# Performance work log

Measured on AMD Instinct MI355X. Metric: run time of the kernel, lower is better.

The kernel has to match this reference:

```python
import jax, jax.numpy as jnp
import numpy as np

NUM_CLASSES = 80
ALPHA = 0.25
GAMMA = 2.0
CONF_T = 0.5
IOU_T = 0.5
N_ANCHORS = 6144


def _pairwise_iou(b):
    # b: [n,4] (x1,y1,x2,y2) -> [n,n] IoU matrix
    area = (b[:, 2] - b[:, 0]) * (b[:, 3] - b[:, 1])
    lt = jnp.maximum(b[:, None, :2], b[None, :, :2])
    rb = jnp.minimum(b[:, None, 2:], b[None, :, 2:])
    wh = jnp.clip(rb - lt, 0.0)
    inter = wh[..., 0] * wh[..., 1]
    return inter / (area[:, None] + area[None, :] - inter)


def _nms(boxes, scores, thr):
    # torchvision-style NMS: returns kept indices in decreasing-score order
    order = jnp.argsort(-scores)
    iou = _pairwise_iou(boxes[order])
    n = boxes.shape[0]
    ar = jnp.arange(n)
    def body(i, supp):
        return supp | ((iou[i] > thr) & (ar > i) & jnp.logical_not(supp[i]))
    supp = jax.lax.fori_loop(0, n, body, jnp.zeros(n, dtype=bool))
    kept_pos = jnp.where(~supp)[0]  # eager: concrete shapes
    return order[kept_pos]


def _make_boxes(tb, floc):
    # tb: [1,1,4] target box; floc: [Nf,2] filtered predicted locations
    # replicates loc_determined with T=1: (tx1*px, ty1*py, tx2*px, ty2*py)
    px, py = floc[:, 0], floc[:, 1]
    return jnp.stack([tb[0, 0, 0] * px, tb[0, 0, 1] * py,
                      tb[0, 0, 2] * px, tb[0, 0, 3] * py], axis=1)


def _smooth_l1_sum(pred, tgt):
    d = jnp.abs(pred - tgt)  # broadcasts [k,C,4] vs [1,1,4]
    return jnp.where(d < 1.0, 0.5 * d * d, d - 0.5).sum()


def setup_inputs() -> dict:
    key = jax.random.key(0)
    k1, k2, k3 = jax.random.split(key, 3)
    locations = jax.random.uniform(k1, (1, N_ANCHORS, 2), dtype=jnp.float32)
    confidences = jax.random.uniform(k2, (1, N_ANCHORS, NUM_CLASSES), dtype=jnp.float32)
    # valid target box (x1<x2, y1<y2) in [0,1]
    target_boxes = jnp.array([[[0.15, 0.2, 0.85, 0.9]]], dtype=jnp.float32)
    target_labels = jax.random.randint(k3, (1,), 0, NUM_CLASSES)
    return {"locations": locations, "confidences": confidences,
            "target_boxes": target_boxes, "target_labels": target_labels}


def reference(locations, confidences, target_boxes, target_labels):
    conf = confidences[0]                       # [N,C]
    scores_max = conf.max(axis=1)
    idx_f = jnp.where(scores_max > CONF_T)[0]   # eager boolean filter
    if idx_f.shape[0] == 0:
        return jnp.float32(0.001)
    floc = locations[0, idx_f, :]               # [Nf,2]
    fconf = conf[idx_f]                         # [Nf,C]
    boxes = _make_boxes(target_boxes, floc)     # [Nf,4] (pred_loc_final)
    score = fconf[:, 0]                         # class-0 score, as in original
    keep = _nms(boxes, score, IOU_T)            # kept indices
    if keep.shape[0] == 0:
        return jnp.float32(0.001)
    matched_loc = boxes[keep]                   # [M,4]
    matched_conf = fconf[keep]                  # [M,C]
    k = target_labels.shape[0]                  # = 1
    topv, topi = jax.lax.top_k(matched_conf.T, k)  # per-class top-k over dim 0
    topv, topi = topv.T, topi.T                 # [k,C]
    pred_bin = (topv[:, 0] > 0.5).astype(jnp.float32)  # [k]
    mloc = matched_loc[topi]                    # [k,C,4]
    loc_loss = _smooth_l1_sum(mloc, target_boxes)
    # F.cross_entropy with 1-D float input/target = probabilities mode, unbatched
    ce = -(target_labels.astype(jnp.float32) * jax.nn.log_softmax(pred_bin)).sum()
    focal = ALPHA * (1.0 - jnp.exp(-ce)) ** GAMMA * ce
    # original bug preserved: num_positives = sum of kept *indices*
    num_pos = keep.sum().astype(jnp.float32)
    return (loc_loss + focal) / num_pos
```

## Files before the change

kernel.cpp:

```cpp
#include <hip/hip_runtime.h>
#include <stdint.h>

#define N_ANCHORS 6144
#define NUM_CLASSES 80
#define NWORDS 96
#define NTILES 24
#define SCAN_B 32
#define ROWSTRIDE 128

__device__ unsigned long long g_mask[(size_t)N_ANCHORS * NWORDS + 64];
__device__ float4 g_sbox[N_ANCHORS];
__device__ int    g_rpart[NTILES][N_ANCHORS];
__device__ int    g_fpart[NTILES][N_ANCHORS];
__device__ int    g_sAnchor[N_ANCHORS];
__device__ int    g_sFi[N_ANCHORS];
__device__ int    g_keptPos[N_ANCHORS];
__device__ int    g_F, g_K, g_np, g_done;
__device__ float  g_loss;

__device__ __forceinline__ float anchor_key(const float* __restrict__ conf, int i, bool& valid) {
    const float4* cp4 = (const float4*)(conf + (size_t)i * NUM_CLASSES);
    float4 v0 = cp4[0];
    float score = v0.x;
    float m = fmaxf(fmaxf(v0.x, v0.y), fmaxf(v0.z, v0.w));
    #pragma unroll
    for (int c = 1; c < NUM_CLASSES / 4; ++c) {
        float4 v = cp4[c];
        m = fmaxf(m, fmaxf(fmaxf(v.x, v.y), fmaxf(v.z, v.w)));
    }
    valid = m > 0.5f;
    return valid ? score : -1.0f;
}

__global__ void __launch_bounds__(256) k_rank(const float* __restrict__ conf) {
    __shared__ float skey[256];
    int y = blockIdx.y;
    int j0 = y * 256;
    bool vj;
    skey[threadIdx.x] = anchor_key(conf, j0 + threadIdx.x, vj);
    int i = blockIdx.x * 256 + threadIdx.x;
    bool vi;
    float ki = anchor_key(conf, i, vi);
    __syncthreads();
    int r = 0, f = 0;
    #pragma unroll 8
    for (int jj = 0; jj < 256; ++jj) {
        float kj = skey[jj];
        int j = j0 + jj;
        bool valid_j = kj >= 0.0f;
        r += (kj > ki) || (kj == ki && j < i && valid_j);
        f += (j < i) && valid_j;
    }
    g_rpart[y][i] = r;
    g_fpart[y][i] = f;
}

__global__ void __launch_bounds__(256) k_scatter(const float* __restrict__ loc,
                                                 const float* __restrict__ conf,
                                                 const float* __restrict__ tb) {
    int i = blockIdx.x * 256 + threadIdx.x;
    bool vi;
    float ki = anchor_key(conf, i, vi);
    (void)ki;
    int r = 0, f = 0;
    #pragma unroll
    for (int y = 0; y < NTILES; ++y) { r += g_rpart[y][i]; f += g_fpart[y][i]; }
    if (vi) {
        float px = loc[2 * i], py = loc[2 * i + 1];
        float4 b;
        b.x = __fmul_rn(tb[0], px);
        b.y = __fmul_rn(tb[1], py);
        b.z = __fmul_rn(tb[2], px);
        b.w = __fmul_rn(tb[3], py);
        g_sbox[r] = b;
        g_sAnchor[r] = i;
        g_sFi[r] = f;
    }
    if (i == N_ANCHORS - 1) g_F = f + (vi ? 1 : 0);
}

__global__ void __launch_bounds__(256) k_mask(void) {
    int wave = (blockIdx.x * 256 + threadIdx.x) >> 6;
    int lane = threadIdx.x & 63;
    if (wave >= N_ANCHORS) return;
    int i = wave;
    float4 bi = g_sbox[i];
    float areai = __fmul_rn(bi.z - bi.x, bi.w - bi.y);
    unsigned long long* row = g_mask + (size_t)i * NWORDS;
    for (int w = (i >> 6); w < NWORDS; ++w) {
        float4 bj = g_sbox[w * 64 + lane];
        float areaj = __fmul_rn(bj.z - bj.x, bj.w - bj.y);
        float lx = fmaxf(bi.x, bj.x), ly = fmaxf(bi.y, bj.y);
        float rx = fminf(bi.z, bj.z), ry = fminf(bi.w, bj.w);
        float iw = fmaxf(rx - lx, 0.0f), ih = fmaxf(ry - ly, 0.0f);
        float inter = __fmul_rn(iw, ih);
        float denom = __fsub_rn(__fadd_rn(areai, areaj), inter);
        float iou = __fdiv_rn(inter, denom);
        unsigned long long bits = __ballot(iou > 0.5f);
        if (lane == 0) row[w] = bits;
    }
}

__global__ void __launch_bounds__(64, 1) k_scan(void) {
    __shared__ alignas(16) unsigned long long rowbuf[SCAN_B][ROWSTRIDE];
    __shared__ int slots[SCAN_B];
    int lane = threadIdx.x;
    int F = g_F;
    if (lane == 0) { g_loss = 0.0f; g_np = 0; g_done = 0; }
    if (lane < SCAN_B) slots[lane] = 0;
    auto initw = [&](int w) -> unsigned long long {
        long long lo = (long long)w * 64, hi = lo + 64;
        if (F <= lo) return ~0ull;
        if (F >= hi) return 0ull;
        return (~0ull) << (F - lo);
    };
    unsigned long long remv0 = initw(lane);
    unsigned long long remv1 = (lane < 32) ? initw(64 + lane) : ~0ull;
    unsigned long long kept0 = 0, kept1 = 0;
    int lastPos = -1;

    while (true) {
        unsigned long long c0 = ~remv0;
        unsigned long long c1 = (lane < 32) ? ~remv1 : 0ull;
        {
            long long lo = (long long)lane << 6;
            if (lastPos >= lo + 63)      c0 = 0ull;
            else if (lastPos >= lo)      c0 &= (~0ull) << (int)(lastPos - lo + 1);
        }
        if (lane < 32) {
            long long lo = (long long)(64 + lane) << 6;
            if (lastPos >= lo + 63)      c1 = 0ull;
            else if (lastPos >= lo)      c1 &= (~0ull) << (int)(lastPos - lo + 1);
        }
        int n0 = __popcll(c0), n1 = __popcll(c1);
        int xp = (n0 << 16) | n1;
        for (int ofs = 1; ofs < 64; ofs <<= 1) {
            int y = __shfl_up(xp, ofs, 64);
            if (lane >= ofs) xp += y;
        }
        int lastxp = __builtin_amdgcn_readlane(xp, 63);
        int tot0 = lastxp >> 16, tot1 = lastxp & 0xffff;
        int total = tot0 + tot1;
        if (total == 0) break;
        int nb = (total < SCAN_B) ? total : SCAN_B;
        int off0 = (xp >> 16) - n0;
        int off1 = tot0 + ((xp & 0xffff) - n1);
        {
            unsigned long long wd = c0; int r = off0;
            while (wd && r < SCAN_B) { int b = __builtin_ctzll(wd); slots[r++] = lane * 64 + b; wd &= wd - 1; }
        }
        if (lane < 32) {
            unsigned long long wd = c1; int r = off1;
            while (wd && r < SCAN_B) { int b = __builtin_ctzll(wd); slots[r++] = (64 + lane) * 64 + b; wd &= wd - 1; }
        }
        __syncthreads();
        int myPos = slots[(lane < SCAN_B) ? lane : 0];
        int myW = myPos >> 6, myB = myPos & 63;

        for (int p = 0; p < nb; ++p) {
            int P = __builtin_amdgcn_readlane(myPos, p);
            const unsigned long long* rp = g_mask + (size_t)P * NWORDS;
            __builtin_amdgcn_global_load_lds((const uint32_t*)rp + lane * 4,
                                             (uint32_t*)&rowbuf[p][0], 16, 0, 0);
        }
        asm volatile("s_waitcnt vmcnt(0)" ::: "memory");
        __builtin_amdgcn_sched_barrier(0);

        uint32_t conflict = 0;
        for (int p0 = 0; p0 < nb; p0 += 8) {
            unsigned long long w[8];
            #pragma unroll
            for (int q = 0; q < 8; ++q) w[q] = rowbuf[p0 + q][myW];
            #pragma unroll
            for (int q = 0; q < 8; ++q)
                if (p0 + q < nb) conflict |= (uint32_t)((w[q] >> myB) & 1ull) << (p0 + q);
        }
        conflict &= (lane < nb) ? ((1u << lane) - 1u) : 0u;

        uint32_t keptm = 0;
        for (int p = 0; p < nb; ++p) {
            uint32_t cp = (uint32_t)__builtin_amdgcn_readlane((int)conflict, p);
            if ((cp & keptm) == 0) keptm |= 1u << p;
        }

        uint32_t km = keptm;
        while (km) {
            int kidx[8]; bool kv[8];
            #pragma unroll
            for (int q = 0; q < 8; ++q) {
                kv[q] = (km != 0);
                kidx[q] = kv[q] ? __builtin_ctz(km) : 0;
                if (km) km &= km - 1;
            }
            unsigned long long a0[8], a1[8];
            #pragma unroll
            for (int q = 0; q < 8; ++q) {
                a0[q] = kv[q] ? rowbuf[kidx[q]][lane] : 0ull;
                a1[q] = (kv[q] && lane < 32) ? rowbuf[kidx[q]][64 + lane] : 0ull;
            }
            #pragma unroll
            for (int q = 0; q < 8; ++q) { remv0 |= a0[q]; if (lane < 32) remv1 |= a1[q]; }
            #pragma unroll
            for (int q = 0; q < 8; ++q) {
                if (kv[q]) {
                    int P = __builtin_amdgcn_readlane(myPos, kidx[q]);
                    int w = P >> 6, b = P & 63;
                    if (w < 64) { if (lane == w) kept0 |= 1ull << b; }
                    else        { if (lane == w - 64) kept1 |= 1ull << b; }
                }
            }
        }
        lastPos = __builtin_amdgcn_readlane(myPos, nb - 1);
    }

    int c0 = __popcll(kept0);
    int c1 = (lane < 32) ? __popcll(kept1) : 0;
    int xp = (c0 << 16) | c1;
    for (int ofs = 1; ofs < 64; ofs <<= 1) {
        int y = __shfl_up(xp, ofs, 64);
        if (lane >= ofs) xp += y;
    }
    int lastxp = __builtin_amdgcn_readlane(xp, 63);
    int t0 = lastxp >> 16, t1 = lastxp & 0xffff;
    int off = (xp >> 16) - c0;
    unsigned long long wd = kept0;
    while (wd) { int b = __builtin_ctzll(wd); g_keptPos[off++] = lane * 64 + b; wd &= wd - 1; }
    off = t0 + ((xp & 0xffff) - c1);
    wd = kept1;
    while (wd) { int b = __builtin_ctzll(wd); g_keptPos[off++] = (64 + lane) * 64 + b; wd &= wd - 1; }
    if (lane == 0) g_K = t0 + t1;
}

__global__ void __launch_bounds__(64) k_loss(const float* __restrict__ conf, const float* __restrict__ tb,
                                             float* __restrict__ out) {
    int c = blockIdx.x;
    int lane = threadIdx.x;
    int K = g_K;
    float bv = -3.402823466e+38f;
    int bk = 0x7fffffff;
    int np = 0;
    for (int k = lane; k < K; k += 64) {
        int p = g_keptPos[k];
        int a = g_sAnchor[p];
        float v = conf[(size_t)a * NUM_CLASSES + c];
        if (v > bv || (v == bv && k < bk)) { bv = v; bk = k; }
        if (c == 0) np += g_sFi[p];
    }
    for (int ofs = 32; ofs > 0; ofs >>= 1) {
        float ov = __shfl_down(bv, ofs, 64);
        int ok = __shfl_down(bk, ofs, 64);
        if (ov > bv || (ov == bv && ok < bk)) { bv = ov; bk = ok; }
    }
    if (c == 0) {
        for (int ofs = 32; ofs > 0; ofs >>= 1) np += __shfl_down(np, ofs, 64);
        if (lane == 0) atomicExch(&g_np, np);
    }
    if (lane == 0) {
        if (K > 0) {
            float4 b = g_sbox[g_keptPos[bk]];
            float t0 = tb[0], t1 = tb[1], t2 = tb[2], t3 = tb[3];
            float l = 0.0f, d;
            d = fabsf(b.x - t0); l += (d < 1.0f) ? 0.5f * d * d : d - 0.5f;
            d = fabsf(b.y - t1); l += (d < 1.0f) ? 0.5f * d * d : d - 0.5f;
            d = fabsf(b.z - t2); l += (d < 1.0f) ? 0.5f * d * d : d - 0.5f;
            d = fabsf(b.w - t3); l += (d < 1.0f) ? 0.5f * d * d : d - 0.5f;
            atomicAdd(&g_loss, l);
        }
        __threadfence();
        int done = atomicAdd(&g_done, 1);
        if (done == NUM_CLASSES - 1) {
            float total = atomicAdd(&g_loss, 0.0f);
            int npv = atomicAdd(&g_np, 0);
            out[0] = (g_F == 0 || K == 0) ? 0.001f : total / (float)npv;
        }
    }
}

extern "C" void kernel_launch(void* const* d_in, const int* in_sizes, int n_in,
                              void* d_out, int out_size, void* d_ws, size_t ws_size,
                              hipStream_t stream) {
    const float* loc  = (const float*)d_in[0];
    const float* conf = (const float*)d_in[1];
    const float* tb   = (const float*)d_in[2];
    float* out = (float*)d_out;

    k_rank<<<dim3(NTILES, NTILES), 256, 0, stream>>>(conf);
    k_scatter<<<NTILES, 256, 0, stream>>>(loc, conf, tb);
    k_mask<<<(N_ANCHORS * 64) / 256, 256, 0, stream>>>();
    k_scan<<<1, 64, 0, stream>>>();
    k_loss<<<NUM_CLASSES, 64, 0, stream>>>(conf, tb, out);
}
```

Before: 167.7 us.

## Load NMS mask rows into registers and recompute intra-batch IoU conflicts

Each candidate-batch step of the serial NMS scan now loads all 32 mask rows straight from global memory into registers, replacing the async global-to-LDS staging buffer. The intra-batch conflict matrix is computed by redoing the IoU between the batch boxes with lane broadcasts instead of reading mask bits from LDS, and the kept-row OR loop is fully unrolled with no LDS reads. The aim is to take LDS round trips and the wait barrier off the latency-bound single-wave scan. In exchange it always issues 32 row loads per step even when the batch is smaller, and adds heavy register pressure from 64 64-bit values.

```diff
diff --git a/kernel.cpp b/kernel.cpp
--- a/kernel.cpp
+++ b/kernel.cpp
@@ -6,7 +6,6 @@
 #define NWORDS 96
 #define NTILES 24
 #define SCAN_B 32
-#define ROWSTRIDE 128
 
 __device__ unsigned long long g_mask[(size_t)N_ANCHORS * NWORDS + 64];
 __device__ float4 g_sbox[N_ANCHORS];
@@ -17,6 +16,10 @@
 __device__ int    g_keptPos[N_ANCHORS];
 __device__ int    g_F, g_K, g_np, g_done;
 __device__ float  g_loss;
+
+__device__ __forceinline__ float rdlf(float v, int l) {
+    return __int_as_float(__builtin_amdgcn_readlane(__float_as_int(v), l));
+}
 
 __device__ __forceinline__ float anchor_key(const float* __restrict__ conf, int i, bool& valid) {
     const float4* cp4 = (const float4*)(conf + (size_t)i * NUM_CLASSES);
@@ -102,7 +105,6 @@
 }
 
 __global__ void __launch_bounds__(64, 1) k_scan(void) {
-    __shared__ alignas(16) unsigned long long rowbuf[SCAN_B][ROWSTRIDE];
     __shared__ int slots[SCAN_B];
     int lane = threadIdx.x;
     int F = g_F;
@@ -154,60 +156,52 @@
             while (wd && r < SCAN_B) { int b = __builtin_ctzll(wd); slots[r++] = (64 + lane) * 64 + b; wd &= wd - 1; }
         }
         __syncthreads();
-        int myPos = slots[(lane < SCAN_B) ? lane : 0];
-        int myW = myPos >> 6, myB = myPos & 63;
-
-        for (int p = 0; p < nb; ++p) {
-            int P = __builtin_amdgcn_readlane(myPos, p);
-            const unsigned long long* rp = g_mask + (size_t)P * NWORDS;
-            __builtin_amdgcn_global_load_lds((const uint32_t*)rp + lane * 4,
-                                             (uint32_t*)&rowbuf[p][0], 16, 0, 0);
-        }
-        asm volatile("s_waitcnt vmcnt(0)" ::: "memory");
-        __builtin_amdgcn_sched_barrier(0);
+        int myPos = slots[lane & 31];
+
+        int Ps[SCAN_B];
+        unsigned long long r0[SCAN_B], r1[SCAN_B];
+        #pragma unroll
+        for (int p = 0; p < SCAN_B; ++p) {
+            Ps[p] = __builtin_amdgcn_readlane(myPos, p);
+            const unsigned long long* rp = g_mask + (size_t)Ps[p] * NWORDS;
+            r0[p] = rp[lane];
+            r1[p] = rp[64 + lane];
+        }
+
+        float4 bj = g_sbox[myPos];
+        float areaj = __fmul_rn(bj.z - bj.x, bj.w - bj.y);
 
         uint32_t conflict = 0;
-        for (int p0 = 0; p0 < nb; p0 += 8) {
-            unsigned long long w[8];
-            #pragma unroll
-            for (int q = 0; q < 8; ++q) w[q] = rowbuf[p0 + q][myW];
-            #pragma unroll
-            for (int q = 0; q < 8; ++q)
-                if (p0 + q < nb) conflict |= (uint32_t)((w[q] >> myB) & 1ull) << (p0 + q);
-        }
+        #pragma unroll
+        for (int p = 0; p < SCAN_B; ++p) {
+            float bix = rdlf(bj.x, p), biy = rdlf(bj.y, p), biz = rdlf(bj.z, p), biw = rdlf(bj.w, p);
+            float areai = __fmul_rn(biz - bix, biw - biy);
+            float lx = fmaxf(bix, bj.x), ly = fmaxf(biy, bj.y);
+            float rx = fminf(biz, bj.z), ry = fminf(biw, bj.w);
+            float iw = fmaxf(rx - lx, 0.0f), ih = fmaxf(ry - ly, 0.0f);
+            float inter = __fmul_rn(iw, ih);
+            float denom = __fsub_rn(__fadd_rn(areai, areaj), inter);
+            float iou = __fdiv_rn(inter, denom);
+            if (iou > 0.5f) conflict |= 1u << p;
+        }
+        conflict &= (nb >= 32) ? 0xffffffffu : ((1u << nb) - 1u);
         conflict &= (lane < nb) ? ((1u << lane) - 1u) : 0u;
 
         uint32_t keptm = 0;
         for (int p = 0; p < nb; ++p) {
             uint32_t cp = (uint32_t)__builtin_amdgcn_readlane((int)conflict, p);
-            if ((cp & keptm) == 0) keptm |= 1u << p;
-        }
-
-        uint32_t km = keptm;
-        while (km) {
-            int kidx[8]; bool kv[8];
-            #pragma unroll
-            for (int q = 0; q < 8; ++q) {
-                kv[q] = (km != 0);
-                kidx[q] = kv[q] ? __builtin_ctz(km) : 0;
-                if (km) km &= km - 1;
-            }
-            unsigned long long a0[8], a1[8];
-            #pragma unroll
-            for (int q = 0; q < 8; ++q) {
-                a0[q] = kv[q] ? rowbuf[kidx[q]][lane] : 0ull;
-                a1[q] = (kv[q] && lane < 32) ? rowbuf[kidx[q]][64 + lane] : 0ull;
-            }
-            #pragma unroll
-            for (int q = 0; q < 8; ++q) { remv0 |= a0[q]; if (lane < 32) remv1 |= a1[q]; }
-            #pragma unroll
-            for (int q = 0; q < 8; ++q) {
-                if (kv[q]) {
-                    int P = __builtin_amdgcn_readlane(myPos, kidx[q]);
-                    int w = P >> 6, b = P & 63;
-                    if (w < 64) { if (lane == w) kept0 |= 1ull << b; }
-                    else        { if (lane == w - 64) kept1 |= 1ull << b; }
-                }
+            if ((cp & keptm) == 0u) keptm |= 1u << p;
+        }
+
+        #pragma unroll
+        for (int p = 0; p < SCAN_B; ++p) {
+            if ((keptm >> p) & 1u) {
+                remv0 |= r0[p];
+                remv1 |= r1[p];
+                int P = Ps[p];
+                int w = P >> 6, b = P & 63;
+                if (w < 64) { if (lane == w) kept0 |= 1ull << b; }
+                else        { if (lane == w - 64) kept1 |= 1ull << b; }
             }
         }
         lastPos = __builtin_amdgcn_readlane(myPos, nb - 1);
```

Result: no change. 167.9 us (+0.1%).
